# Kernel tuning notes

Hardware: AMD Instinct MI355X
Metric: run time of the kernel (lower is better)

## Reference

```python
import jax, jax.numpy as jnp
import numpy as np

NUM_HEADS = 16
NEG_BIG = -1e9


def setup_inputs() -> dict:
    key = jax.random.key(0)
    ks = jax.random.split(key, 5)
    B, S, D = 8, 1024, 1024
    x = jax.random.normal(ks[0], (B, S, D), dtype=jnp.float32)
    # binary mask (1 = masked position), shape (B, 1, S, S) per docstring
    mask = (jax.random.uniform(ks[1], (B, 1, S, S)) < 0.5).astype(jnp.float32)
    W_attn = jax.random.normal(ks[2], (D, 3 * D), dtype=jnp.float32) * (1.0 / np.sqrt(D))
    b_attn = jnp.zeros((3 * D,), dtype=jnp.float32)
    W_proj = jax.random.normal(ks[3], (D, D), dtype=jnp.float32) * (1.0 / np.sqrt(D))
    b_proj = jnp.zeros((D,), dtype=jnp.float32)
    return {"x": x, "mask": mask, "W_attn": W_attn, "b_attn": b_attn,
            "W_proj": W_proj, "b_proj": b_proj}


def reference(x, mask, W_attn, b_attn, W_proj, b_proj):
    B, S, D = x.shape
    H = NUM_HEADS
    dh = D // H
    # c_attn: fused qkv projection (1x1 conv == linear)
    qkv = x @ W_attn + b_attn                      # [B, S, 3D]
    q, k, v = jnp.split(qkv, 3, axis=-1)
    # split heads -> [B, H, S, dh]
    def split_heads(t):
        return t.reshape(B, S, H, dh).transpose(0, 2, 1, 3)
    q, k, v = split_heads(q), split_heads(k), split_heads(v)
    # scaled dot-product scores
    scores = jnp.einsum("bhqd,bhkd->bhqk", q, k) / jnp.sqrt(jnp.asarray(dh, x.dtype))
    # NOTE: source applies mask multiplicatively: scores * (mask * -1e9)
    scores = scores * (mask * NEG_BIG)
    attn = jax.nn.softmax(scores, axis=-1)         # [B, H, S, S]
    # eval mode: dropout disabled
    out = jnp.einsum("bhqk,bhkd->bhqd", attn, v)   # [B, H, S, dh]
    out = out.transpose(0, 2, 1, 3).reshape(B, S, D)
    # c_proj (residual dropout disabled in eval)
    return out @ W_proj + b_proj
```

## Files before the change

kernel.cpp:

```cpp
#include <hip/hip_runtime.h>
#include <math.h>


typedef double f64x4 __attribute__((ext_vector_type(4)));

__device__ int g_qk_mode;

__global__ void qk_calib(const float* __restrict__ X, const float* __restrict__ W)
{
  __shared__ double As[16][66];
  __shared__ double Bs[16][66];
  const int t = threadIdx.x;
  const int lm = t & 15, l4 = t >> 4;
  for (int p = 0; p < 16; ++p) {
    int f = p * 64 + t;
    int k = f >> 6, m = f & 63;
    As[k][m] = (double)X[(size_t)m * 1024 + k];
    Bs[k][m] = (double)W[(size_t)k * 3072 + m];
  }
  __syncthreads();
  f64x4 acc = {0., 0., 0., 0.};
#pragma unroll
  for (int k0 = 0; k0 < 16; k0 += 4) {
    double a = As[k0 + l4][lm];
    double b = Bs[k0 + l4][lm];
    acc = __builtin_amdgcn_mfma_f64_16x16x4f64(a, b, acc, 0, 0, 0);
  }
  double ref00 = 0., ref01 = 0., ref10 = 0., ref40 = 0., ref04 = 0.;
#pragma unroll
  for (int kk = 0; kk < 16; ++kk) {
    double a0 = As[kk][0], a1 = As[kk][1], a4 = As[kk][4];
    double b0 = Bs[kk][0], b1 = Bs[kk][1], b4 = Bs[kk][4];
    ref00 = fma(a0, b0, ref00);
    ref01 = fma(a0, b1, ref01);
    ref10 = fma(a1, b0, ref10);
    ref40 = fma(a4, b0, ref40);
    ref04 = fma(a0, b4, ref04);
  }
  double v00 = __shfl(acc[0], 0);
  double v16 = __shfl(acc[0], 16);
  if (t == 0) {
    int m;
    if (fabs(v00 - ref00) > 1e-5) {
      m = 0;
    } else {
      double d1 = fabs(v16 - ref40);
      double d2 = fabs(v16 - ref10);
      double d3 = fabs(v16 - ref04);
      double d4 = fabs(v16 - ref01);
      m = 1; double best = d1;
      if (d2 < best) { best = d2; m = 2; }
      if (d3 < best) { best = d3; m = 3; }
      if (d4 < best) { best = d4; m = 4; }
    }
    g_qk_mode = m;
  }
}

__global__ __launch_bounds__(256) void qk_gemm_f64(
    const float* __restrict__ X, const float* __restrict__ W,
    const float* __restrict__ bias,
    double* __restrict__ qT, double* __restrict__ kT, int b0)
{
  __shared__ double As[16][66];
  __shared__ double Bs[16][66];
  const int t = threadIdx.x;
  const int lane = t & 63, w = t >> 6;
  const int lm = lane & 15, l4 = lane >> 4;
  const int m0w = (w & 1) * 32, n0w = (w >> 1) * 32;
  const int n0 = blockIdx.x * 64;
  const int m0 = blockIdx.y * 64;
  const int mode = g_qk_mode;
  f64x4 acc00 = {0.,0.,0.,0.}, acc01 = {0.,0.,0.,0.};
  f64x4 acc10 = {0.,0.,0.,0.}, acc11 = {0.,0.,0.,0.};
  const size_t xrow0 = (size_t)b0 * 1024 + m0;

  if (mode != 0) {
    for (int k0t = 0; k0t < 1024; k0t += 16) {
      __syncthreads();
      {
        int r = t >> 2, kq = (t & 3) << 2;
        float4 xv = *(const float4*)&X[(xrow0 + r) * 1024 + k0t + kq];
        As[kq + 0][r] = (double)xv.x;
        As[kq + 1][r] = (double)xv.y;
        As[kq + 2][r] = (double)xv.z;
        As[kq + 3][r] = (double)xv.w;
        int kr = t >> 4, cq = (t & 15) << 2;
        float4 wv = *(const float4*)&W[(size_t)(k0t + kr) * 3072 + n0 + cq];
        Bs[kr][cq + 0] = (double)wv.x;
        Bs[kr][cq + 1] = (double)wv.y;
        Bs[kr][cq + 2] = (double)wv.z;
        Bs[kr][cq + 3] = (double)wv.w;
      }
      __syncthreads();
#pragma unroll
      for (int k0 = 0; k0 < 16; k0 += 4) {
        double a0 = As[k0 + l4][m0w + lm];
        double a1 = As[k0 + l4][m0w + 16 + lm];
        double bb0 = Bs[k0 + l4][n0w + lm];
        double bb1 = Bs[k0 + l4][n0w + 16 + lm];
        acc00 = __builtin_amdgcn_mfma_f64_16x16x4f64(a0, bb0, acc00, 0, 0, 0);
        acc01 = __builtin_amdgcn_mfma_f64_16x16x4f64(a0, bb1, acc01, 0, 0, 0);
        acc10 = __builtin_amdgcn_mfma_f64_16x16x4f64(a1, bb0, acc10, 0, 0, 0);
        acc11 = __builtin_amdgcn_mfma_f64_16x16x4f64(a1, bb1, acc11, 0, 0, 0);
      }
    }
  }

  double* T = (n0 < 1024) ? qT : kT;
  const int nn = n0 & 1023;
  const int h = nn >> 6;
  const int bl = m0 >> 10;
  const int sb = m0 & 1023;
  const size_t hb = (size_t)(bl * 16 + h) * 64;

  if (mode != 0) {
#pragma unroll
    for (int ni = 0; ni < 2; ++ni) {
#pragma unroll
      for (int mi = 0; mi < 2; ++mi) {
        f64x4 av = ni ? (mi ? acc11 : acc01) : (mi ? acc10 : acc00);
        if (mode <= 2) {
          const int d = n0w + 16 * ni + lm;
          const double bz = (double)bias[n0 + d];
          const size_t cb = ((hb + d) << 10) + sb;
#pragma unroll
          for (int r = 0; r < 4; ++r) {
            int row = m0w + 16 * mi + ((mode == 1) ? (4 * l4 + r) : (l4 + 4 * r));
            T[cb + row] = av[r] + bz;
          }
        } else {
          const int row = m0w + 16 * mi + lm;
#pragma unroll
          for (int r = 0; r < 4; ++r) {
            int d = n0w + 16 * ni + ((mode == 3) ? (4 * l4 + r) : (l4 + 4 * r));
            T[((hb + d) << 10) + sb + row] = av[r] + (double)bias[n0 + d];
          }
        }
      }
    }
  } else {
    double accv[2][8];
#pragma unroll
    for (int i = 0; i < 2; ++i)
#pragma unroll
      for (int j = 0; j < 8; ++j) accv[i][j] = 0.;
    for (int k0t = 0; k0t < 1024; k0t += 16) {
      __syncthreads();
      {
        int r = t >> 2, kq = (t & 3) << 2;
        float4 xv = *(const float4*)&X[(xrow0 + r) * 1024 + k0t + kq];
        As[kq + 0][r] = (double)xv.x;
        As[kq + 1][r] = (double)xv.y;
        As[kq + 2][r] = (double)xv.z;
        As[kq + 3][r] = (double)xv.w;
        int kr = t >> 4, cq = (t & 15) << 2;
        float4 wv = *(const float4*)&W[(size_t)(k0t + kr) * 3072 + n0 + cq];
        Bs[kr][cq + 0] = (double)wv.x;
        Bs[kr][cq + 1] = (double)wv.y;
        Bs[kr][cq + 2] = (double)wv.z;
        Bs[kr][cq + 3] = (double)wv.w;
      }
      __syncthreads();
#pragma unroll
      for (int kk = 0; kk < 16; ++kk) {
        double a0 = As[kk][m0w + lm];
        double a1 = As[kk][m0w + 16 + lm];
#pragma unroll
        for (int j = 0; j < 8; ++j) {
          double bb = Bs[kk][n0w + 8 * l4 + j];
          accv[0][j] = fma(a0, bb, accv[0][j]);
          accv[1][j] = fma(a1, bb, accv[1][j]);
        }
      }
    }
#pragma unroll
    for (int j = 0; j < 8; ++j) {
      const int d = n0w + 8 * l4 + j;
      const double bz = (double)bias[n0 + d];
      const size_t cb = ((hb + d) << 10) + sb;
      T[cb + m0w + lm]      = accv[0][j] + bz;
      T[cb + m0w + 16 + lm] = accv[1][j] + bz;
    }
  }
}

__global__ __launch_bounds__(256) void v_gemm_f32(
    const float* __restrict__ X, const float* __restrict__ W,
    const float* __restrict__ bias, float* __restrict__ Vp, int b0)
{
  __shared__ __align__(16) float As[16][132];
  __shared__ __align__(16) float Bs[16][132];
  const int t = threadIdx.x, tx = t & 15, ty = t >> 4;
  const int n0 = blockIdx.x * 128;
  const int m0 = blockIdx.y * 128;
  float acc[2][2][4][4] = {};
  const size_t xrow0 = (size_t)b0 * 1024 + m0;

  for (int k0 = 0; k0 < 1024; k0 += 16) {
    __syncthreads();
#pragma unroll
    for (int p = 0; p < 2; ++p) {
      int f = p * 256 + t;
      int r = f >> 2, kq = (f & 3) << 2;
      float4 xv = *(const float4*)&X[(xrow0 + r) * 1024 + k0 + kq];
      As[kq + 0][r] = xv.x; As[kq + 1][r] = xv.y;
      As[kq + 2][r] = xv.z; As[kq + 3][r] = xv.w;
      int kr = f >> 5, cq = (f & 31) << 2;
      *(float4*)&Bs[kr][cq] = *(const float4*)&W[(size_t)(k0 + kr) * 3072 + 2048 + n0 + cq];
    }
    __syncthreads();
#pragma unroll
    for (int kk = 0; kk < 16; ++kk) {
      float4 A0 = *(const float4*)&As[kk][4 * ty];
      float4 A1 = *(const float4*)&As[kk][64 + 4 * ty];
      float4 B0 = *(const float4*)&Bs[kk][4 * tx];
      float4 B1 = *(const float4*)&Bs[kk][64 + 4 * tx];
      float a[2][4] = {{A0.x, A0.y, A0.z, A0.w}, {A1.x, A1.y, A1.z, A1.w}};
      float b[2][4] = {{B0.x, B0.y, B0.z, B0.w}, {B1.x, B1.y, B1.z, B1.w}};
#pragma unroll
      for (int ri = 0; ri < 2; ++ri)
#pragma unroll
        for (int i = 0; i < 4; ++i)
#pragma unroll
          for (int ci = 0; ci < 2; ++ci)
#pragma unroll
            for (int j = 0; j < 4; ++j)
              acc[ri][ci][i][j] = fmaf(a[ri][i], b[ci][j], acc[ri][ci][i][j]);
    }
  }
  const int bl = m0 >> 10;
  const int sb = m0 & 1023;
#pragma unroll
  for (int ci = 0; ci < 2; ++ci) {
    int h = (n0 >> 6) + ci;
    float bz[4];
#pragma unroll
    for (int j = 0; j < 4; ++j) bz[j] = bias[2048 + n0 + 64 * ci + 4 * tx + j];
#pragma unroll
    for (int ri = 0; ri < 2; ++ri)
#pragma unroll
      for (int i = 0; i < 4; ++i) {
        int s = sb + 64 * ri + 4 * ty + i;
        float4 vv = make_float4(acc[ri][ci][i][0] + bz[0], acc[ri][ci][i][1] + bz[1],
                                acc[ri][ci][i][2] + bz[2], acc[ri][ci][i][3] + bz[3]);
        *(float4*)&Vp[((size_t)(bl * 16 + h) * 1024 + s) * 64 + 4 * tx] = vv;
      }
  }
}

__global__ __launch_bounds__(256) void attn_fused(
    const double* __restrict__ qT, const double* __restrict__ kT,
    const float* __restrict__ Vp, const float* __restrict__ Mask,
    float* __restrict__ AO, int b0)
{
  __shared__ double Qs[64][64];
  __shared__ double KVd[64][64];
  const int t = threadIdx.x, tx = t & 15, ty = t >> 4;
  const int bh = blockIdx.y;
  const int bl = bh >> 4, h = bh & 15;
  const int bg = b0 + bl;
  const int q0 = blockIdx.x * 64;
  const double* qTb = qT + (size_t)bh * 65536;
  const double* kTb = kT + (size_t)bh * 65536;
  const float*  Vb  = Vp + (size_t)bh * 65536;
  const float*  mb  = Mask + (size_t)bg * 1048576 + (size_t)q0 * 1024;
  float* Ps = (float*)&KVd[0][0];
  float* Vf = (float*)((char*)&KVd[0][0] + 16384);

#pragma unroll
  for (int p = 0; p < 8; ++p) {
    int f = p * 256 + t;
    int d = f >> 5, c = f & 31;
    *(double2*)&Qs[d][2 * c] = *(const double2*)&qTb[(size_t)d * 1024 + q0 + 2 * c];
  }

  double Mreg[4] = {-1e300, -1e300, -1e300, -1e300};
  float Lreg[4] = {0.f, 0.f, 0.f, 0.f};
  float o[4][4] = {};

  for (int kt = 0; kt < 16; ++kt) {
    const int k0 = kt * 64;
    __syncthreads();
#pragma unroll
    for (int p = 0; p < 8; ++p) {
      int f = p * 256 + t;
      int d = f >> 5, c = f & 31;
      *(double2*)&KVd[d][2 * c] = *(const double2*)&kTb[(size_t)d * 1024 + k0 + 2 * c];
    }
    __syncthreads();
    double s[4][4] = {};
#pragma unroll 4
    for (int d = 0; d < 64; ++d) {
      double2 qa = *(const double2*)&Qs[d][2 * ty];
      double2 qb = *(const double2*)&Qs[d][2 * ty + 32];
      double2 ka = *(const double2*)&KVd[d][2 * tx];
      double2 kb = *(const double2*)&KVd[d][2 * tx + 32];
      double aq[4] = {qa.x, qa.y, qb.x, qb.y};
      double ak[4] = {ka.x, ka.y, kb.x, kb.y};
#pragma unroll
      for (int i = 0; i < 4; ++i)
#pragma unroll
        for (int j = 0; j < 4; ++j)
          s[i][j] = fma(aq[i], ak[j], s[i][j]);
    }
    __syncthreads();
    float al[4];
#pragma unroll
    for (int i = 0; i < 4; ++i) {
      const int qi = 2 * ty + (i & 1) + (i >> 1) * 32;
      float2 m01 = *(const float2*)&mb[(size_t)qi * 1024 + k0 + 2 * tx];
      float2 m23 = *(const float2*)&mb[(size_t)qi * 1024 + k0 + 2 * tx + 32];
      double z0 = (m01.x != 0.f) ? s[i][0] * -1.25e8 : 0.0;
      double z1 = (m01.y != 0.f) ? s[i][1] * -1.25e8 : 0.0;
      double z2 = (m23.x != 0.f) ? s[i][2] * -1.25e8 : 0.0;
      double z3 = (m23.y != 0.f) ? s[i][3] * -1.25e8 : 0.0;
      double mx = fmax(fmax(z0, z1), fmax(z2, z3));
#pragma unroll
      for (int ww = 1; ww < 16; ww <<= 1) mx = fmax(mx, __shfl_xor(mx, ww));
      double nM = fmax(Mreg[i], mx);
      double da = Mreg[i] - nM;
      al[i] = (da < -80.0) ? 0.f : expf((float)da);
      double d0 = z0 - nM, d1 = z1 - nM, d2 = z2 - nM, d3 = z3 - nM;
      float p0 = (d0 < -80.0) ? 0.f : expf((float)d0);
      float p1 = (d1 < -80.0) ? 0.f : expf((float)d1);
      float p2 = (d2 < -80.0) ? 0.f : expf((float)d2);
      float p3 = (d3 < -80.0) ? 0.f : expf((float)d3);
      float ps = ((p0 + p1) + p2) + p3;
#pragma unroll
      for (int ww = 1; ww < 16; ww <<= 1) ps += __shfl_xor(ps, ww);
      Lreg[i] = Lreg[i] * al[i] + ps;
      Mreg[i] = nM;
      *(float2*)&Ps[qi * 64 + 2 * tx] = make_float2(p0, p1);
      *(float2*)&Ps[qi * 64 + 2 * tx + 32] = make_float2(p2, p3);
    }
#pragma unroll
    for (int p = 0; p < 4; ++p) {
      int f = p * 256 + t;
      *(float4*)&Vf[4 * f] = *(const float4*)&Vb[(size_t)k0 * 64 + 4 * f];
    }
    __syncthreads();
#pragma unroll
    for (int i = 0; i < 4; ++i) {
      o[i][0] *= al[i]; o[i][1] *= al[i]; o[i][2] *= al[i]; o[i][3] *= al[i];
    }
#pragma unroll 4
    for (int kk = 0; kk < 64; kk += 4) {
      float4 vv0 = *(const float4*)&Vf[(kk + 0) * 64 + 4 * tx];
      float4 vv1 = *(const float4*)&Vf[(kk + 1) * 64 + 4 * tx];
      float4 vv2 = *(const float4*)&Vf[(kk + 2) * 64 + 4 * tx];
      float4 vv3 = *(const float4*)&Vf[(kk + 3) * 64 + 4 * tx];
#pragma unroll
      for (int i = 0; i < 4; ++i) {
        const int qi = 2 * ty + (i & 1) + (i >> 1) * 32;
        float4 pa = *(const float4*)&Ps[qi * 64 + kk];
        o[i][0] = fmaf(pa.x, vv0.x, o[i][0]);
        o[i][0] = fmaf(pa.y, vv1.x, o[i][0]);
        o[i][0] = fmaf(pa.z, vv2.x, o[i][0]);
        o[i][0] = fmaf(pa.w, vv3.x, o[i][0]);
        o[i][1] = fmaf(pa.x, vv0.y, o[i][1]);
        o[i][1] = fmaf(pa.y, vv1.y, o[i][1]);
        o[i][1] = fmaf(pa.z, vv2.y, o[i][1]);
        o[i][1] = fmaf(pa.w, vv3.y, o[i][1]);
        o[i][2] = fmaf(pa.x, vv0.z, o[i][2]);
        o[i][2] = fmaf(pa.y, vv1.z, o[i][2]);
        o[i][2] = fmaf(pa.z, vv2.z, o[i][2]);
        o[i][2] = fmaf(pa.w, vv3.z, o[i][2]);
        o[i][3] = fmaf(pa.x, vv0.w, o[i][3]);
        o[i][3] = fmaf(pa.y, vv1.w, o[i][3]);
        o[i][3] = fmaf(pa.z, vv2.w, o[i][3]);
        o[i][3] = fmaf(pa.w, vv3.w, o[i][3]);
      }
    }
  }
#pragma unroll
  for (int i = 0; i < 4; ++i) {
    const int qi = 2 * ty + (i & 1) + (i >> 1) * 32;
    float inv = (Lreg[i] > 0.f) ? 1.f / Lreg[i] : 0.f;
    float4 vv = make_float4(o[i][0] * inv, o[i][1] * inv, o[i][2] * inv, o[i][3] * inv);
    *(float4*)&AO[(size_t)(bl * 1024 + q0 + qi) * 1024 + h * 64 + 4 * tx] = vv;
  }
}

__global__ __launch_bounds__(256) void proj_gemm(
    const float* __restrict__ AO, const float* __restrict__ W,
    const float* __restrict__ bias, float* __restrict__ Out, int b0)
{
  __shared__ __align__(16) float As[16][132];
  __shared__ __align__(16) float Bs[16][132];
  const int t = threadIdx.x, tx = t & 15, ty = t >> 4;
  const int n0 = blockIdx.x * 128;
  const int m0l = blockIdx.y * 128;
  float acc[2][2][4][4] = {};

  for (int k0 = 0; k0 < 1024; k0 += 16) {
    __syncthreads();
#pragma unroll
    for (int p = 0; p < 2; ++p) {
      int f = p * 256 + t;
      int r = f >> 2, kq = (f & 3) << 2;
      float4 av = *(const float4*)&AO[(size_t)(m0l + r) * 1024 + k0 + kq];
      As[kq + 0][r] = av.x; As[kq + 1][r] = av.y;
      As[kq + 2][r] = av.z; As[kq + 3][r] = av.w;
      int kr = f >> 5, cq = (f & 31) << 2;
      *(float4*)&Bs[kr][cq] = *(const float4*)&W[(size_t)(k0 + kr) * 1024 + n0 + cq];
    }
    __syncthreads();
#pragma unroll
    for (int kk = 0; kk < 16; ++kk) {
      float4 A0 = *(const float4*)&As[kk][4 * ty];
      float4 A1 = *(const float4*)&As[kk][64 + 4 * ty];
      float4 B0 = *(const float4*)&Bs[kk][4 * tx];
      float4 B1 = *(const float4*)&Bs[kk][64 + 4 * tx];
      float a[2][4] = {{A0.x, A0.y, A0.z, A0.w}, {A1.x, A1.y, A1.z, A1.w}};
      float b[2][4] = {{B0.x, B0.y, B0.z, B0.w}, {B1.x, B1.y, B1.z, B1.w}};
#pragma unroll
      for (int ri = 0; ri < 2; ++ri)
#pragma unroll
        for (int i = 0; i < 4; ++i)
#pragma unroll
          for (int ci = 0; ci < 2; ++ci)
#pragma unroll
            for (int j = 0; j < 4; ++j)
              acc[ri][ci][i][j] = fmaf(a[ri][i], b[ci][j], acc[ri][ci][i][j]);
    }
  }
#pragma unroll
  for (int ci = 0; ci < 2; ++ci) {
    float bz[4];
#pragma unroll
    for (int j = 0; j < 4; ++j) bz[j] = bias[n0 + 64 * ci + 4 * tx + j];
#pragma unroll
    for (int ri = 0; ri < 2; ++ri)
#pragma unroll
      for (int i = 0; i < 4; ++i) {
        float4 vv = make_float4(acc[ri][ci][i][0] + bz[0], acc[ri][ci][i][1] + bz[1],
                                acc[ri][ci][i][2] + bz[2], acc[ri][ci][i][3] + bz[3]);
        size_t row = (size_t)b0 * 1024 + m0l + 64 * ri + 4 * ty + i;
        *(float4*)&Out[row * 1024 + n0 + 64 * ci + 4 * tx] = vv;
      }
  }
}

extern "C" void kernel_launch(void* const* d_in, const int* in_sizes, int n_in,
                              void* d_out, int out_size, void* d_ws, size_t ws_size,
                              hipStream_t stream) {
  (void)in_sizes; (void)n_in; (void)out_size;
  const float* x      = (const float*)d_in[0];
  const float* mask   = (const float*)d_in[1];
  const float* W_attn = (const float*)d_in[2];
  const float* b_attn = (const float*)d_in[3];
  const float* W_proj = (const float*)d_in[4];
  const float* b_proj = (const float*)d_in[5];
  float* out = (float*)d_out;

  int CB = (ws_size >= (192ull << 20)) ? 8
         : (ws_size >= (96ull  << 20)) ? 4
         : (ws_size >= (48ull  << 20)) ? 2 : 1;

  char* base = (char*)d_ws;
  double* qT = (double*)base;
  double* kT = (double*)(base + (size_t)CB * (8ull  << 20));
  float*  Vp = (float*)(base + (size_t)CB * (16ull << 20));
  float*  AO = (float*)(base + (size_t)CB * (20ull << 20));

  qk_calib<<<1, 64, 0, stream>>>(x, W_attn);
  for (int b0 = 0; b0 < 8; b0 += CB) {
    qk_gemm_f64<<<dim3(32, 16 * CB), 256, 0, stream>>>(x, W_attn, b_attn, qT, kT, b0);
    v_gemm_f32<<<dim3(8, 8 * CB), 256, 0, stream>>>(x, W_attn, b_attn, Vp, b0);
    attn_fused<<<dim3(16, 16 * CB), 256, 0, stream>>>(qT, kT, Vp, mask, AO, b0);
    proj_gemm<<<dim3(8, 8 * CB), 256, 0, stream>>>(AO, W_proj, b_proj, out, b0);
  }
}
```

Before: 1.794 ms.

## Use FP64 MFMA for QK scores in attention with 32-row query tiles

Computes the double-precision QK^T scores in the fused attention kernel with the MFMA f64 16x16x4 instruction. Q fragments are held in registers and the accumulator layout is selected at runtime through the calibrated g_qk_mode flag, with a scalar fallback when the mode is zero. Query tiles shrink from 64 to 32 rows, so the grid doubles and less shared memory is used per block. Scores are staged through padded LDS so the softmax and PV stages keep their thread mapping. The cost is extra LDS round trips and barriers, and K/V tiles are now reloaded for twice as many blocks.

```diff
diff --git a/kernel.cpp b/kernel.cpp
--- a/kernel.cpp
+++ b/kernel.cpp
@@ -254,30 +254,35 @@
     const float* __restrict__ Vp, const float* __restrict__ Mask,
     float* __restrict__ AO, int b0)
 {
-  __shared__ double Qs[64][64];
-  __shared__ double KVd[64][64];
-  const int t = threadIdx.x, tx = t & 15, ty = t >> 4;
+  __shared__ double KVd[64][66];
+  __shared__ float  Ps[32][66];
+  double* Sd = &KVd[0][0];
+  float*  Vf = (float*)((char*)&KVd[0][0] + 16896);
+
+  const int t = threadIdx.x;
+  const int lane = t & 63, w = t >> 6;
+  const int lm = lane & 15, l4 = lane >> 4;
+  const int tx = t & 15, ty = t >> 4;
   const int bh = blockIdx.y;
   const int bl = bh >> 4, h = bh & 15;
   const int bg = b0 + bl;
-  const int q0 = blockIdx.x * 64;
+  const int q0 = blockIdx.x * 32;
   const double* qTb = qT + (size_t)bh * 65536;
   const double* kTb = kT + (size_t)bh * 65536;
   const float*  Vb  = Vp + (size_t)bh * 65536;
   const float*  mb  = Mask + (size_t)bg * 1048576 + (size_t)q0 * 1024;
-  float* Ps = (float*)&KVd[0][0];
-  float* Vf = (float*)((char*)&KVd[0][0] + 16384);
-
-#pragma unroll
-  for (int p = 0; p < 8; ++p) {
-    int f = p * 256 + t;
-    int d = f >> 5, c = f & 31;
-    *(double2*)&Qs[d][2 * c] = *(const double2*)&qTb[(size_t)d * 1024 + q0 + 2 * c];
-  }
-
-  double Mreg[4] = {-1e300, -1e300, -1e300, -1e300};
-  float Lreg[4] = {0.f, 0.f, 0.f, 0.f};
-  float o[4][4] = {};
+  const int mode = g_qk_mode;
+
+  double qreg[2][16];
+#pragma unroll
+  for (int qt = 0; qt < 2; ++qt)
+#pragma unroll
+    for (int s = 0; s < 16; ++s)
+      qreg[qt][s] = qTb[(size_t)(4 * s + l4) * 1024 + q0 + 16 * qt + lm];
+
+  double Mreg[2] = {-1e300, -1e300};
+  float Lreg[2] = {0.f, 0.f};
+  float o[2][4] = {};
 
   for (int kt = 0; kt < 16; ++kt) {
     const int k0 = kt * 64;
@@ -289,59 +294,109 @@
       *(double2*)&KVd[d][2 * c] = *(const double2*)&kTb[(size_t)d * 1024 + k0 + 2 * c];
     }
     __syncthreads();
-    double s[4][4] = {};
-#pragma unroll 4
-    for (int d = 0; d < 64; ++d) {
-      double2 qa = *(const double2*)&Qs[d][2 * ty];
-      double2 qb = *(const double2*)&Qs[d][2 * ty + 32];
-      double2 ka = *(const double2*)&KVd[d][2 * tx];
-      double2 kb = *(const double2*)&KVd[d][2 * tx + 32];
-      double aq[4] = {qa.x, qa.y, qb.x, qb.y};
-      double ak[4] = {ka.x, ka.y, kb.x, kb.y};
-#pragma unroll
-      for (int i = 0; i < 4; ++i)
+
+    f64x4 acc0 = {0., 0., 0., 0.}, acc1 = {0., 0., 0., 0.};
+    double sv[2][4];
+    if (mode != 0) {
+#pragma unroll
+      for (int s = 0; s < 16; ++s) {
+        double b = KVd[4 * s + l4][16 * w + lm];
+        acc0 = __builtin_amdgcn_mfma_f64_16x16x4f64(qreg[0][s], b, acc0, 0, 0, 0);
+        acc1 = __builtin_amdgcn_mfma_f64_16x16x4f64(qreg[1][s], b, acc1, 0, 0, 0);
+      }
+    } else {
+#pragma unroll
+      for (int i = 0; i < 2; ++i)
+#pragma unroll
+        for (int j = 0; j < 4; ++j) sv[i][j] = 0.;
+      for (int d = 0; d < 64; ++d) {
+        double qv0 = qTb[(size_t)d * 1024 + q0 + 2 * ty];
+        double qv1 = qTb[(size_t)d * 1024 + q0 + 2 * ty + 1];
+#pragma unroll
+        for (int j = 0; j < 4; ++j) {
+          double kv = KVd[d][tx + 16 * j];
+          sv[0][j] = fma(qv0, kv, sv[0][j]);
+          sv[1][j] = fma(qv1, kv, sv[1][j]);
+        }
+      }
+    }
+    __syncthreads();
+
+    if (mode != 0) {
+      const int nof = 16 * w;
+#pragma unroll
+      for (int qt = 0; qt < 2; ++qt) {
+        f64x4 av = qt ? acc1 : acc0;
+        if (mode <= 2) {
+          const int k = nof + lm;
+#pragma unroll
+          for (int r = 0; r < 4; ++r) {
+            int q = 16 * qt + ((mode == 1) ? (4 * l4 + r) : (l4 + 4 * r));
+            Sd[k * 33 + q] = av[r];
+          }
+        } else {
+          const int q = 16 * qt + lm;
+#pragma unroll
+          for (int r = 0; r < 4; ++r) {
+            int k = nof + ((mode == 3) ? (4 * l4 + r) : (l4 + 4 * r));
+            Sd[k * 33 + q] = av[r];
+          }
+        }
+      }
+    } else {
+#pragma unroll
+      for (int i = 0; i < 2; ++i)
 #pragma unroll
         for (int j = 0; j < 4; ++j)
-          s[i][j] = fma(aq[i], ak[j], s[i][j]);
-    }
-    __syncthreads();
-    float al[4];
-#pragma unroll
-    for (int i = 0; i < 4; ++i) {
-      const int qi = 2 * ty + (i & 1) + (i >> 1) * 32;
-      float2 m01 = *(const float2*)&mb[(size_t)qi * 1024 + k0 + 2 * tx];
-      float2 m23 = *(const float2*)&mb[(size_t)qi * 1024 + k0 + 2 * tx + 32];
-      double z0 = (m01.x != 0.f) ? s[i][0] * -1.25e8 : 0.0;
-      double z1 = (m01.y != 0.f) ? s[i][1] * -1.25e8 : 0.0;
-      double z2 = (m23.x != 0.f) ? s[i][2] * -1.25e8 : 0.0;
-      double z3 = (m23.y != 0.f) ? s[i][3] * -1.25e8 : 0.0;
-      double mx = fmax(fmax(z0, z1), fmax(z2, z3));
+          Sd[(tx + 16 * j) * 33 + 2 * ty + i] = sv[i][j];
+    }
+#pragma unroll
+    for (int p = 0; p < 4; ++p) {
+      int f = p * 256 + t;
+      *(float4*)&Vf[4 * f] = *(const float4*)&Vb[(size_t)k0 * 64 + 4 * f];
+    }
+    __syncthreads();
+
+    float al[2];
+#pragma unroll
+    for (int i = 0; i < 2; ++i) {
+      const int q = 2 * ty + i;
+      double z[4];
+#pragma unroll
+      for (int j = 0; j < 4; ++j) {
+        int k = tx + 16 * j;
+        double s = Sd[k * 33 + q];
+        float mv = mb[(size_t)q * 1024 + k0 + k];
+        z[j] = (mv != 0.f) ? s * -1.25e8 : 0.0;
+      }
+      double mx = fmax(fmax(z[0], z[1]), fmax(z[2], z[3]));
 #pragma unroll
       for (int ww = 1; ww < 16; ww <<= 1) mx = fmax(mx, __shfl_xor(mx, ww));
       double nM = fmax(Mreg[i], mx);
       double da = Mreg[i] - nM;
       al[i] = (da < -80.0) ? 0.f : expf((float)da);
-      double d0 = z0 - nM, d1 = z1 - nM, d2 = z2 - nM, d3 = z3 - nM;
-      float p0 = (d0 < -80.0) ? 0.f : expf((float)d0);
-      float p1 = (d1 < -80.0) ? 0.f : expf((float)d1);
-      float p2 = (d2 < -80.0) ? 0.f : expf((float)d2);
-      float p3 = (d3 < -80.0) ? 0.f : expf((float)d3);
+      float p0, p1, p2, p3;
+      {
+        double d0 = z[0] - nM, d1 = z[1] - nM, d2 = z[2] - nM, d3 = z[3] - nM;
+        p0 = (d0 < -80.0) ? 0.f : expf((float)d0);
+        p1 = (d1 < -80.0) ? 0.f : expf((float)d1);
+        p2 = (d2 < -80.0) ? 0.f : expf((float)d2);
+        p3 = (d3 < -80.0) ? 0.f : expf((float)d3);
+      }
       float ps = ((p0 + p1) + p2) + p3;
 #pragma unroll
       for (int ww = 1; ww < 16; ww <<= 1) ps += __shfl_xor(ps, ww);
       Lreg[i] = Lreg[i] * al[i] + ps;
       Mreg[i] = nM;
-      *(float2*)&Ps[qi * 64 + 2 * tx] = make_float2(p0, p1);
-      *(float2*)&Ps[qi * 64 + 2 * tx + 32] = make_float2(p2, p3);
-    }
-#pragma unroll
-    for (int p = 0; p < 4; ++p) {
-      int f = p * 256 + t;
-      *(float4*)&Vf[4 * f] = *(const float4*)&Vb[(size_t)k0 * 64 + 4 * f];
-    }
-    __syncthreads();
-#pragma unroll
-    for (int i = 0; i < 4; ++i) {
+      Ps[q][tx +  0] = p0;
+      Ps[q][tx + 16] = p1;
+      Ps[q][tx + 32] = p2;
+      Ps[q][tx + 48] = p3;
+    }
+    __syncthreads();
+
+#pragma unroll
+    for (int i = 0; i < 2; ++i) {
       o[i][0] *= al[i]; o[i][1] *= al[i]; o[i][2] *= al[i]; o[i][3] *= al[i];
     }
 #pragma unroll 4
@@ -351,34 +406,37 @@
       float4 vv2 = *(const float4*)&Vf[(kk + 2) * 64 + 4 * tx];
       float4 vv3 = *(const float4*)&Vf[(kk + 3) * 64 + 4 * tx];
 #pragma unroll
-      for (int i = 0; i < 4; ++i) {
-        const int qi = 2 * ty + (i & 1) + (i >> 1) * 32;
-        float4 pa = *(const float4*)&Ps[qi * 64 + kk];
-        o[i][0] = fmaf(pa.x, vv0.x, o[i][0]);
-        o[i][0] = fmaf(pa.y, vv1.x, o[i][0]);
-        o[i][0] = fmaf(pa.z, vv2.x, o[i][0]);
-        o[i][0] = fmaf(pa.w, vv3.x, o[i][0]);
-        o[i][1] = fmaf(pa.x, vv0.y, o[i][1]);
-        o[i][1] = fmaf(pa.y, vv1.y, o[i][1]);
-        o[i][1] = fmaf(pa.z, vv2.y, o[i][1]);
-        o[i][1] = fmaf(pa.w, vv3.y, o[i][1]);
-        o[i][2] = fmaf(pa.x, vv0.z, o[i][2]);
-        o[i][2] = fmaf(pa.y, vv1.z, o[i][2]);
-        o[i][2] = fmaf(pa.z, vv2.z, o[i][2]);
-        o[i][2] = fmaf(pa.w, vv3.z, o[i][2]);
-        o[i][3] = fmaf(pa.x, vv0.w, o[i][3]);
-        o[i][3] = fmaf(pa.y, vv1.w, o[i][3]);
-        o[i][3] = fmaf(pa.z, vv2.w, o[i][3]);
-        o[i][3] = fmaf(pa.w, vv3.w, o[i][3]);
-      }
-    }
-  }
-#pragma unroll
-  for (int i = 0; i < 4; ++i) {
-    const int qi = 2 * ty + (i & 1) + (i >> 1) * 32;
+      for (int i = 0; i < 2; ++i) {
+        const int q = 2 * ty + i;
+        float pa0 = Ps[q][kk + 0];
+        float pa1 = Ps[q][kk + 1];
+        float pa2 = Ps[q][kk + 2];
+        float pa3 = Ps[q][kk + 3];
+        o[i][0] = fmaf(pa0, vv0.x, o[i][0]);
+        o[i][0] = fmaf(pa1, vv1.x, o[i][0]);
+        o[i][0] = fmaf(pa2, vv2.x, o[i][0]);
+        o[i][0] = fmaf(pa3, vv3.x, o[i][0]);
+        o[i][1] = fmaf(pa0, vv0.y, o[i][1]);
+        o[i][1] = fmaf(pa1, vv1.y, o[i][1]);
+        o[i][1] = fmaf(pa2, vv2.y, o[i][1]);
+        o[i][1] = fmaf(pa3, vv3.y, o[i][1]);
+        o[i][2] = fmaf(pa0, vv0.z, o[i][2]);
+        o[i][2] = fmaf(pa1, vv1.z, o[i][2]);
+        o[i][2] = fmaf(pa2, vv2.z, o[i][2]);
+        o[i][2] = fmaf(pa3, vv3.z, o[i][2]);
+        o[i][3] = fmaf(pa0, vv0.w, o[i][3]);
+        o[i][3] = fmaf(pa1, vv1.w, o[i][3]);
+        o[i][3] = fmaf(pa2, vv2.w, o[i][3]);
+        o[i][3] = fmaf(pa3, vv3.w, o[i][3]);
+      }
+    }
+  }
+#pragma unroll
+  for (int i = 0; i < 2; ++i) {
+    const int q = 2 * ty + i;
     float inv = (Lreg[i] > 0.f) ? 1.f / Lreg[i] : 0.f;
     float4 vv = make_float4(o[i][0] * inv, o[i][1] * inv, o[i][2] * inv, o[i][3] * inv);
-    *(float4*)&AO[(size_t)(bl * 1024 + q0 + qi) * 1024 + h * 64 + 4 * tx] = vv;
+    *(float4*)&AO[(size_t)(bl * 1024 + q0 + q) * 1024 + h * 64 + 4 * tx] = vv;
   }
 }
 
@@ -468,7 +526,7 @@
   for (int b0 = 0; b0 < 8; b0 += CB) {
     qk_gemm_f64<<<dim3(32, 16 * CB), 256, 0, stream>>>(x, W_attn, b_attn, qT, kT, b0);
     v_gemm_f32<<<dim3(8, 8 * CB), 256, 0, stream>>>(x, W_attn, b_attn, Vp, b0);
-    attn_fused<<<dim3(16, 16 * CB), 256, 0, stream>>>(qT, kT, Vp, mask, AO, b0);
+    attn_fused<<<dim3(32, 16 * CB), 256, 0, stream>>>(qT, kT, Vp, mask, AO, b0);
     proj_gemm<<<dim3(8, 8 * CB), 256, 0, stream>>>(AO, W_proj, b_proj, out, b0);
   }
 }
```

Measured after the change: 1.862 ms. +3.8%, slower.
